# Optimization experiments

Hardware: AMD Instinct MI355X
Metric: run time of the kernel (lower is better)

The kernel has to match this reference:

```python
import jax, jax.numpy as jnp
import numpy as np


def setup_inputs() -> dict:
    key = jax.random.key(0)
    k1, k2 = jax.random.split(key)
    s = jax.random.normal(k1, (8192, 512), dtype=jnp.float32)
    t = jax.random.normal(k2, (8192, 512), dtype=jnp.float32)
    return {"s": s, "t": t}


def reference(s, t):
    # Pairwise squared Euclidean distance: dist[i, j] = ||t[j] - s[i]||^2
    # Expressed via the identity ||s||^2 + ||t||^2 - 2 s @ t^T to avoid
    # materializing the [n, q, d] broadcast intermediate of the original.
    s_sq = jnp.sum(s * s, axis=1)  # [n]
    t_sq = jnp.sum(t * t, axis=1)  # [q]
    cross = jnp.einsum('nd,qd->nq', s, t)  # [n, q]
    dist = s_sq[:, None] + t_sq[None, :] - 2.0 * cross
    return dist
```

## Files before the change

kernel.cpp:

```cpp
#include <hip/hip_runtime.h>
#include <hip/hip_bf16.h>
#include <stdint.h>


typedef __attribute__((ext_vector_type(8))) short short8v;
typedef __attribute__((ext_vector_type(4))) float f32x4;

static __device__ __forceinline__ unsigned short f32_to_bf16_rne(float f) {
    unsigned int u = __float_as_uint(f);
    unsigned int lsb = (u >> 16) & 1u;
    u += 0x7fffu + lsb;
    return (unsigned short)(u >> 16);
}

static __device__ __forceinline__ void async_load16(const void* g, void* l) {
    __builtin_amdgcn_global_load_lds(
        (const __attribute__((address_space(1))) void*)g,
        (__attribute__((address_space(3))) void*)l,
        16, 0, 0);
}

__global__ __launch_bounds__(256) void prep_kernel(const float* __restrict__ x,
                                                   unsigned short* __restrict__ xb,
                                                   float* __restrict__ nrm,
                                                   float scale) {
    const int tid  = threadIdx.x;
    const int wid  = tid >> 6;
    const int lane = tid & 63;
    const int row  = blockIdx.x * 4 + wid;
    const float* xr = x + (size_t)row * 512;

    float4 v0 = ((const float4*)xr)[lane * 2 + 0];
    float4 v1 = ((const float4*)xr)[lane * 2 + 1];

    float ss = v0.x * v0.x + v0.y * v0.y + v0.z * v0.z + v0.w * v0.w
             + v1.x * v1.x + v1.y * v1.y + v1.z * v1.z + v1.w * v1.w;
#pragma unroll
    for (int off = 32; off > 0; off >>= 1) ss += __shfl_down(ss, off, 64);
    if (lane == 0) nrm[row] = ss;

    unsigned short u[8];
    float vals[8] = {v0.x, v0.y, v0.z, v0.w, v1.x, v1.y, v1.z, v1.w};
#pragma unroll
    for (int e = 0; e < 8; ++e) u[e] = f32_to_bf16_rne(vals[e] * scale);
    unsigned int w0 = (unsigned)u[0] | ((unsigned)u[1] << 16);
    unsigned int w1 = (unsigned)u[2] | ((unsigned)u[3] << 16);
    unsigned int w2 = (unsigned)u[4] | ((unsigned)u[5] << 16);
    unsigned int w3 = (unsigned)u[6] | ((unsigned)u[7] << 16);
    uint4 pk = make_uint4(w0, w1, w2, w3);
    ((uint4*)(xb + (size_t)row * 512))[lane] = pk;
}

#define BM 256
#define BK 32
#define NSLOT 4

__global__ __launch_bounds__(512, 2) void dist_mfma(const unsigned short* __restrict__ sb,
                                                    const unsigned short* __restrict__ tb,
                                                    const float* __restrict__ ssq,
                                                    const float* __restrict__ tsq,
                                                    float* __restrict__ out,
                                                    int N, int Q, int D) {
    __shared__ __align__(16) unsigned short lds[2 * NSLOT * 256 * 32];

    const int tid  = threadIdx.x;
    const int wid  = tid >> 6;
    const int lane = tid & 63;
    const int quad = lane >> 4;
    const int r    = lane & 15;
    const int wr   = wid >> 2;
    const int wc   = wid & 3;
    const int m_w  = wr * 128;
    const int n_w  = wc * 64;

    const int bid = blockIdx.x;
    const int nBm = N / BM, nBn = Q / BM;
    int bm, bn;
    if ((nBm & 7) == 0 && (nBn & 7) == 0) {
        const int super = bid >> 6, within = bid & 63;
        const int spr = nBn >> 3;
        const int sm = super / spr, sn = super % spr;
        bm = (sm << 3) + (within >> 3);
        bn = (sn << 3) + (within & 7);
    } else {
        bm = bid / nBn;
        bn = bid - bm * nBn;
    }

    f32x4 acc[8][4];
#pragma unroll
    for (int a = 0; a < 8; ++a)
#pragma unroll
        for (int b = 0; b < 4; ++b) acc[a][b] = (f32x4){0.f, 0.f, 0.f, 0.f};

    const unsigned short* gA[2];
    const unsigned short* gB[2];
    unsigned short* lA[2];
    unsigned short* lB[2];
#pragma unroll
    for (int i = 0; i < 2; ++i) {
        const int p   = i * 512 + tid;
        const int row = p >> 2;
        const int gch = (p & 3) ^ (row & 3);
        gA[i] = sb + (size_t)(bm * BM + row) * D + gch * 8;
        gB[i] = tb + (size_t)(bn * BM + row) * D + gch * 8;
        lA[i] = lds + (i * 512 + wid * 64) * 8;
        lB[i] = lds + NSLOT * 8192 + (i * 512 + wid * 64) * 8;
    }

#define STAGE(t, s) do { const int k0_ = (t) * BK;                  \
        async_load16(gA[0] + k0_, lA[0] + (s) * 8192);              \
        async_load16(gB[0] + k0_, lB[0] + (s) * 8192);              \
        async_load16(gA[1] + k0_, lA[1] + (s) * 8192);              \
        async_load16(gB[1] + k0_, lB[1] + (s) * 8192); } while (0)

    STAGE(0, 0);
    STAGE(1, 1);

    const int NT = D / BK;
    for (int t = 0; t < NT; ++t) {
        if (t + 2 < NT) STAGE(t + 2, (t + 2) & 3);
        if (t < NT - 2) {
            asm volatile("s_waitcnt vmcnt(8) lgkmcnt(0)" ::: "memory");
        } else if (t == NT - 2) {
            asm volatile("s_waitcnt vmcnt(4) lgkmcnt(0)" ::: "memory");
        } else {
            asm volatile("s_waitcnt vmcnt(0) lgkmcnt(0)" ::: "memory");
        }
        __builtin_amdgcn_sched_barrier(0);
        __builtin_amdgcn_s_barrier();
        __builtin_amdgcn_sched_barrier(0);

        const unsigned short* ba = lds + (t & 3) * 8192;
        const unsigned short* bb = lds + NSLOT * 8192 + (t & 3) * 8192;
        short8v aF[8], bF[4];
#pragma unroll
        for (int im = 0; im < 8; ++im) {
            const int row = m_w + im * 16 + r;
            const int cp  = quad ^ (row & 3);
            aF[im] = *(const short8v*)(ba + row * 32 + cp * 8);
        }
#pragma unroll
        for (int in = 0; in < 4; ++in) {
            const int row = n_w + in * 16 + r;
            const int cp  = quad ^ (row & 3);
            bF[in] = *(const short8v*)(bb + row * 32 + cp * 8);
        }
        __builtin_amdgcn_s_setprio(1);
#pragma unroll
        for (int im = 0; im < 8; ++im)
#pragma unroll
            for (int in = 0; in < 4; ++in)
                acc[im][in] = __builtin_amdgcn_mfma_f32_16x16x32_bf16(
                    aF[im], bF[in], acc[im][in], 0, 0, 0);
        __builtin_amdgcn_s_setprio(0);
    }
#undef STAGE

    const int gm = bm * BM + m_w;
    const int gn = bn * BM + n_w;
    float tq[4];
#pragma unroll
    for (int in = 0; in < 4; ++in) tq[in] = tsq[gn + in * 16 + r];
#pragma unroll
    for (int im = 0; im < 8; ++im) {
#pragma unroll
        for (int j = 0; j < 4; ++j) {
            const int i = gm + im * 16 + quad * 4 + j;
            const float sv = ssq[i];
            float* orow = out + (size_t)i * (size_t)Q + gn;
#pragma unroll
            for (int in = 0; in < 4; ++in)
                __builtin_nontemporal_store(sv + tq[in] + acc[im][in][j],
                                            &orow[in * 16 + r]);
        }
    }
}

__global__ void dist_fallback(const float* __restrict__ s, const float* __restrict__ t,
                              float* __restrict__ out, int N, int Q, int D) {
    __shared__ float ls[16][17], lt[16][17];
    const int tj = threadIdx.x, ti = threadIdx.y;
    const int i = blockIdx.y * 16 + ti, j = blockIdx.x * 16 + tj;
    float cross = 0.f, ssq = 0.f, tsq = 0.f;
    for (int k0 = 0; k0 < D; k0 += 16) {
        __syncthreads();
        ls[ti][tj] = s[(size_t)(blockIdx.y * 16 + ti) * D + k0 + tj];
        lt[ti][tj] = t[(size_t)(blockIdx.x * 16 + ti) * D + k0 + tj];
        __syncthreads();
#pragma unroll
        for (int kk = 0; kk < 16; ++kk) {
            float a = ls[ti][kk], b = lt[tj][kk];
            cross += a * b; ssq += a * a; tsq += b * b;
        }
    }
    out[(size_t)i * Q + j] = ssq + tsq - 2.f * cross;
}

extern "C" void kernel_launch(void* const* d_in, const int* in_sizes, int n_in,
                              void* d_out, int out_size, void* d_ws, size_t ws_size,
                              hipStream_t stream) {
    const float* s = (const float*)d_in[0];
    const float* t = (const float*)d_in[1];
    float* out = (float*)d_out;
    const int D = 512;
    const int N = in_sizes[0] / D;
    const int Q = in_sizes[1] / D;

    const size_t need = ((size_t)N + (size_t)Q) * D * sizeof(unsigned short)
                      + ((size_t)N + (size_t)Q) * sizeof(float);

    if (ws_size >= need && D == 512 && (N % BM) == 0 && (Q % BM) == 0) {
        unsigned short* sb = (unsigned short*)d_ws;
        unsigned short* tb = sb + (size_t)N * D;
        float* ssq = (float*)(tb + (size_t)Q * D);
        float* tsq = ssq + N;
        prep_kernel<<<N / 4, 256, 0, stream>>>(s, sb, ssq, -2.0f);
        prep_kernel<<<Q / 4, 256, 0, stream>>>(t, tb, tsq, 1.0f);
        const int blocks = (N / BM) * (Q / BM);
        dist_mfma<<<blocks, 512, 0, stream>>>(sb, tb, ssq, tsq, out, N, Q, D);
    } else {
        dim3 g(Q / 16, N / 16), b(16, 16);
        dist_fallback<<<g, b, 0, stream>>>(s, t, out, N, Q, D);
    }
}
```

Before: 370.6 us.

## Restructure MFMA mainloop into BK64 double-buffered quadrant schedule with interleaved loads

Raises the K tile from 32 to 64 and switches from a 4-slot ring to a double buffer split into four half-tiles (A lo/hi, B lo/hi). The MFMA work is split into four quadrant phases, each loading part of the fragments and issuing the async global-to-LDS load for one half of the next tile, with barriers and priority bumps around each phase. It also moves to an 8-way XOR swizzle for the 64-wide rows. The aim is to overlap global loads with matrix math more finely and to halve the number of K iterations. The cost is more barriers per tile and tighter vmcnt bookkeeping.

```diff
diff --git a/kernel.cpp b/kernel.cpp
--- a/kernel.cpp
+++ b/kernel.cpp
@@ -52,8 +52,9 @@
 }
 
 #define BM 256
-#define BK 32
-#define NSLOT 4
+#define BKT 64
+#define NTILE 8
+
 
 __global__ __launch_bounds__(512, 2) void dist_mfma(const unsigned short* __restrict__ sb,
                                                     const unsigned short* __restrict__ tb,
@@ -61,7 +62,7 @@
                                                     const float* __restrict__ tsq,
                                                     float* __restrict__ out,
                                                     int N, int Q, int D) {
-    __shared__ __align__(16) unsigned short lds[2 * NSLOT * 256 * 32];
+    __shared__ __align__(16) unsigned short lds[2 * 32768];
 
     const int tid  = threadIdx.x;
     const int wid  = tid >> 6;
@@ -70,8 +71,6 @@
     const int r    = lane & 15;
     const int wr   = wid >> 2;
     const int wc   = wid & 3;
-    const int m_w  = wr * 128;
-    const int n_w  = wc * 64;
 
     const int bid = blockIdx.x;
     const int nBm = N / BM, nBn = Q / BM;
@@ -93,72 +92,134 @@
 #pragma unroll
         for (int b = 0; b < 4; ++b) acc[a][b] = (f32x4){0.f, 0.f, 0.f, 0.f};
 
-    const unsigned short* gA[2];
-    const unsigned short* gB[2];
-    unsigned short* lA[2];
-    unsigned short* lB[2];
+    const unsigned short* gH[4][2];
 #pragma unroll
     for (int i = 0; i < 2; ++i) {
-        const int p   = i * 512 + tid;
-        const int row = p >> 2;
-        const int gch = (p & 3) ^ (row & 3);
-        gA[i] = sb + (size_t)(bm * BM + row) * D + gch * 8;
-        gB[i] = tb + (size_t)(bn * BM + row) * D + gch * 8;
-        lA[i] = lds + (i * 512 + wid * 64) * 8;
-        lB[i] = lds + NSLOT * 8192 + (i * 512 + wid * 64) * 8;
-    }
-
-#define STAGE(t, s) do { const int k0_ = (t) * BK;                  \
-        async_load16(gA[0] + k0_, lA[0] + (s) * 8192);              \
-        async_load16(gB[0] + k0_, lB[0] + (s) * 8192);              \
-        async_load16(gA[1] + k0_, lA[1] + (s) * 8192);              \
-        async_load16(gB[1] + k0_, lB[1] + (s) * 8192); } while (0)
-
-    STAGE(0, 0);
-    STAGE(1, 1);
-
-    const int NT = D / BK;
-    for (int t = 0; t < NT; ++t) {
-        if (t + 2 < NT) STAGE(t + 2, (t + 2) & 3);
-        if (t < NT - 2) {
-            asm volatile("s_waitcnt vmcnt(8) lgkmcnt(0)" ::: "memory");
-        } else if (t == NT - 2) {
-            asm volatile("s_waitcnt vmcnt(4) lgkmcnt(0)" ::: "memory");
-        } else {
-            asm volatile("s_waitcnt vmcnt(0) lgkmcnt(0)" ::: "memory");
+        const int row = (i * 512 + tid) >> 3;
+        const int gch = (tid ^ row) & 7;
+        gH[0][i] = sb + (size_t)(bm * BM +       row) * 512 + gch * 8;
+        gH[1][i] = sb + (size_t)(bm * BM + 128 + row) * 512 + gch * 8;
+        gH[2][i] = tb + (size_t)(bn * BM +       row) * 512 + gch * 8;
+        gH[3][i] = tb + (size_t)(bn * BM + 128 + row) * 512 + gch * 8;
+    }
+    const int ldsl = tid * 8;
+
+#define STAGE_HALF(h, t, b) do {                                              \
+        async_load16(gH[h][0] + (t) * BKT,                                    \
+                     lds + (b) * 32768 + (h) * 8192 + ldsl);                  \
+        async_load16(gH[h][1] + (t) * BKT,                                    \
+                     lds + (b) * 32768 + (h) * 8192 + 4096 + ldsl);           \
+    } while (0)
+
+    const int aBase = (wr * 128 + r) * 64;
+    const int bBase = 16384 + (wc * 64 + r) * 64;
+    int cSw[2];
+#pragma unroll
+    for (int kk = 0; kk < 2; ++kk) cSw[kk] = ((kk * 4 + quad) ^ (r & 7)) * 8;
+
+    STAGE_HALF(0, 0, 0); STAGE_HALF(1, 0, 0);
+    STAGE_HALF(2, 0, 0); STAGE_HALF(3, 0, 0);
+    STAGE_HALF(0, 1, 1);
+    asm volatile("s_waitcnt vmcnt(2)" ::: "memory");
+    __builtin_amdgcn_s_barrier();
+
+#define SYNC_PRE() do {                                                       \
+        __builtin_amdgcn_s_barrier();                                         \
+        asm volatile("s_waitcnt lgkmcnt(0)" ::: "memory");                    \
+        __builtin_amdgcn_sched_barrier(0);                                    \
+        __builtin_amdgcn_s_setprio(1);                                        \
+    } while (0)
+#define SYNC_POST() do {                                                      \
+        __builtin_amdgcn_s_setprio(0);                                        \
+        __builtin_amdgcn_s_barrier();                                         \
+    } while (0)
+
+    short8v aF[4][2], bF[4][2];
+
+#pragma unroll 2
+    for (int t = 0; t < NTILE; ++t) {
+        const int b = t & 1;
+        const unsigned short* bufA = lds + b * 32768;
+
+#pragma unroll
+        for (int im = 0; im < 4; ++im)
+#pragma unroll
+            for (int kk = 0; kk < 2; ++kk)
+                aF[im][kk] = *(const short8v*)(bufA + aBase + im * 1024 + cSw[kk]);
+#pragma unroll
+        for (int in = 0; in < 2; ++in)
+#pragma unroll
+            for (int kk = 0; kk < 2; ++kk)
+                bF[in][kk] = *(const short8v*)(bufA + bBase + in * 1024 + cSw[kk]);
+        if (t + 1 < NTILE) STAGE_HALF(1, t + 1, b ^ 1);
+        SYNC_PRE();
+#pragma unroll
+        for (int im = 0; im < 4; ++im)
+#pragma unroll
+            for (int in = 0; in < 2; ++in)
+#pragma unroll
+                for (int kk = 0; kk < 2; ++kk)
+                    acc[im][in] = __builtin_amdgcn_mfma_f32_16x16x32_bf16(
+                        aF[im][kk], bF[in][kk], acc[im][in], 0, 0, 0);
+        SYNC_POST();
+
+#pragma unroll
+        for (int in = 0; in < 2; ++in)
+#pragma unroll
+            for (int kk = 0; kk < 2; ++kk)
+                bF[2 + in][kk] = *(const short8v*)(bufA + bBase + (2 + in) * 1024 + cSw[kk]);
+        if (t + 1 < NTILE) STAGE_HALF(2, t + 1, b ^ 1);
+        SYNC_PRE();
+#pragma unroll
+        for (int im = 0; im < 4; ++im)
+#pragma unroll
+            for (int in = 0; in < 2; ++in)
+#pragma unroll
+                for (int kk = 0; kk < 2; ++kk)
+                    acc[im][2 + in] = __builtin_amdgcn_mfma_f32_16x16x32_bf16(
+                        aF[im][kk], bF[2 + in][kk], acc[im][2 + in], 0, 0, 0);
+        SYNC_POST();
+
+#pragma unroll
+        for (int im = 0; im < 4; ++im)
+#pragma unroll
+            for (int kk = 0; kk < 2; ++kk)
+                aF[im][kk] = *(const short8v*)(bufA + aBase + 4096 + im * 1024 + cSw[kk]);
+        if (t + 1 < NTILE) STAGE_HALF(3, t + 1, b ^ 1);
+        SYNC_PRE();
+#pragma unroll
+        for (int im = 0; im < 4; ++im)
+#pragma unroll
+            for (int in = 0; in < 2; ++in)
+#pragma unroll
+                for (int kk = 0; kk < 2; ++kk)
+                    acc[4 + im][in] = __builtin_amdgcn_mfma_f32_16x16x32_bf16(
+                        aF[im][kk], bF[in][kk], acc[4 + im][in], 0, 0, 0);
+        SYNC_POST();
+
+        if (t + 2 < NTILE) STAGE_HALF(0, t + 2, b);
+        if (t < NTILE - 2) {
+            asm volatile("s_waitcnt vmcnt(2)" ::: "memory");
+        } else if (t == NTILE - 2) {
+            asm volatile("s_waitcnt vmcnt(0)" ::: "memory");
         }
-        __builtin_amdgcn_sched_barrier(0);
-        __builtin_amdgcn_s_barrier();
-        __builtin_amdgcn_sched_barrier(0);
-
-        const unsigned short* ba = lds + (t & 3) * 8192;
-        const unsigned short* bb = lds + NSLOT * 8192 + (t & 3) * 8192;
-        short8v aF[8], bF[4];
-#pragma unroll
-        for (int im = 0; im < 8; ++im) {
-            const int row = m_w + im * 16 + r;
-            const int cp  = quad ^ (row & 3);
-            aF[im] = *(const short8v*)(ba + row * 32 + cp * 8);
-        }
-#pragma unroll
-        for (int in = 0; in < 4; ++in) {
-            const int row = n_w + in * 16 + r;
-            const int cp  = quad ^ (row & 3);
-            bF[in] = *(const short8v*)(bb + row * 32 + cp * 8);
-        }
-        __builtin_amdgcn_s_setprio(1);
-#pragma unroll
-        for (int im = 0; im < 8; ++im)
-#pragma unroll
-            for (int in = 0; in < 4; ++in)
-                acc[im][in] = __builtin_amdgcn_mfma_f32_16x16x32_bf16(
-                    aF[im], bF[in], acc[im][in], 0, 0, 0);
-        __builtin_amdgcn_s_setprio(0);
-    }
-#undef STAGE
-
-    const int gm = bm * BM + m_w;
-    const int gn = bn * BM + n_w;
+        SYNC_PRE();
+#pragma unroll
+        for (int im = 0; im < 4; ++im)
+#pragma unroll
+            for (int in = 0; in < 2; ++in)
+#pragma unroll
+                for (int kk = 0; kk < 2; ++kk)
+                    acc[4 + im][2 + in] = __builtin_amdgcn_mfma_f32_16x16x32_bf16(
+                        aF[im][kk], bF[2 + in][kk], acc[4 + im][2 + in], 0, 0, 0);
+        SYNC_POST();
+    }
+#undef STAGE_HALF
+#undef SYNC_PRE
+#undef SYNC_POST
+
+    const int gm = bm * BM + wr * 128;
+    const int gn = bn * BM + wc * 64;
     float tq[4];
 #pragma unroll
     for (int in = 0; in < 4; ++in) tq[in] = tsq[gn + in * 16 + r];
```

New measurement: 359.4 us. -3.0%, faster.
